# Performance work log

Measured on AMD Instinct MI355X. Metric: run time of the kernel, lower is better.

The kernel has to match this reference:

```python
import jax, jax.numpy as jnp
from jax import lax
import numpy as np

B, T, E, H = 64, 512, 1024, 1024

def setup_inputs() -> dict:
    key = jax.random.key(0)
    k1, k2, k3, k4, k5, k6 = jax.random.split(key, 6)
    s = 1.0 / np.sqrt(H)  # torch LSTM init scale
    embeddings = jax.random.normal(k1, (B, T, E), dtype=jnp.float32)
    seq_lengths = jax.random.randint(k2, (B,), 1, T + 1)
    W_ih = jax.random.uniform(k3, (4 * H, E), minval=-s, maxval=s, dtype=jnp.float32)
    W_hh = jax.random.uniform(k4, (4 * H, H), minval=-s, maxval=s, dtype=jnp.float32)
    b_ih = jax.random.uniform(k5, (4 * H,), minval=-s, maxval=s, dtype=jnp.float32)
    b_hh = jax.random.uniform(k6, (4 * H,), minval=-s, maxval=s, dtype=jnp.float32)
    return {"embeddings": embeddings, "seq_lengths": seq_lengths,
            "W_ih": W_ih, "W_hh": W_hh, "b_ih": b_ih, "b_hh": b_hh}

def _lstm_outputs(embeddings, W_ih, W_hh, b_ih, b_hh):
    x = jnp.swapaxes(embeddings, 0, 1)  # [T, B, E] (time-major, as nn.LSTM batch_first=False)
    # Hoist the input projection into one big GEMM: [T,B,4H]
    x_proj = jnp.einsum('tbe,ge->tbg', x, W_ih) + b_ih + b_hh

    def step(carry, xp):
        h, c = carry
        gates = xp + h @ W_hh.T                      # [B, 4H]
        i, f, g, o = jnp.split(gates, 4, axis=-1)    # torch gate order: i, f, g, o
        i = jax.nn.sigmoid(i)
        f = jax.nn.sigmoid(f)
        g = jnp.tanh(g)
        o = jax.nn.sigmoid(o)
        c = f * c + i * g
        h = o * jnp.tanh(c)
        return (h, c), h

    h0 = jnp.zeros((x.shape[1], W_hh.shape[1]), x.dtype)
    _, outs = lax.scan(step, (h0, h0), x_proj)       # outs: [T, B, H]
    return outs

def reference(embeddings, seq_lengths, W_ih, W_hh, b_ih, b_hh):
    outs = _lstm_outputs(embeddings, W_ih, W_hh, b_ih, b_hh)  # [T, B, H]
    t = outs.shape[0]
    idx = (seq_lengths - 1) % t                      # wraps like python negative indexing
    repr_ = outs[idx, jnp.arange(outs.shape[1])]     # [B, H]
    return repr_
```

## Files before the change

kernel.cpp:

```cpp
#include <hip/hip_runtime.h>
#include <stdint.h>


typedef _Float16 half8 __attribute__((ext_vector_type(8)));
typedef _Float16 half4_ __attribute__((ext_vector_type(4)));
typedef float f32x4 __attribute__((ext_vector_type(4)));
typedef unsigned int u32x4 __attribute__((ext_vector_type(4)));

#define T_SEQ 512

__global__ void k_f32_to_f16(const float* __restrict__ s, _Float16* __restrict__ d, int n4) {
  int i = blockIdx.x * blockDim.x + threadIdx.x;
  if (i >= n4) return;
  f32x4 v = ((const f32x4*)s)[i];
  half4_ h;
  h.x = (_Float16)v.x; h.y = (_Float16)v.y; h.z = (_Float16)v.z; h.w = (_Float16)v.w;
  ((half4_*)d)[i] = h;
}

__global__ void k_bias_sum(const float* __restrict__ a, const float* __restrict__ b,
                           float* __restrict__ o) {
  int i = blockIdx.x * blockDim.x + threadIdx.x;
  if (i < 4096) o[i] = a[i] + b[i];
}

__global__ __launch_bounds__(256, 2) void k_gemm_xproj(
    const _Float16* __restrict__ X, const _Float16* __restrict__ W,
    const float* __restrict__ bsum, _Float16* __restrict__ C) {
  __shared__ _Float16 As[128 * 64];
  __shared__ _Float16 Bs[128 * 64];
  const int bid = blockIdx.x;
  const int ntile = bid & 31, mtile = bid >> 5;
  const int tid = threadIdx.x;
  const int wave = tid >> 6, lane = tid & 63;
  const int wr = wave >> 1, wc = wave & 1;
  const int R0 = lane >> 3, cg = lane & 7;

  f32x4 acc[4][4];
#pragma unroll
  for (int m = 0; m < 4; m++)
#pragma unroll
    for (int n = 0; n < 4; n++) acc[m][n] = (f32x4){0.f, 0.f, 0.f, 0.f};

  for (int k0 = 0; k0 < 1024; k0 += 64) {
#pragma unroll
    for (int i = 0; i < 4; i++) {
      const int rr = (wave * 4 + i) * 8 + R0;
      const _Float16* ga = X + (size_t)(mtile * 128 + rr) * 1024 + k0 + ((cg ^ (rr & 7)) * 8);
      const _Float16* gb = W + (size_t)(ntile * 128 + rr) * 1024 + k0 + ((cg ^ (rr & 7)) * 8);
      __builtin_amdgcn_global_load_lds(
          (const __attribute__((address_space(1))) void*)ga,
          (__attribute__((address_space(3))) void*)((char*)As + (wave * 4 + i) * 1024), 16, 0, 0);
      __builtin_amdgcn_global_load_lds(
          (const __attribute__((address_space(1))) void*)gb,
          (__attribute__((address_space(3))) void*)((char*)Bs + (wave * 4 + i) * 1024), 16, 0, 0);
    }
    asm volatile("s_waitcnt vmcnt(0)" ::: "memory");
    __syncthreads();
#pragma unroll
    for (int kk = 0; kk < 2; kk++) {
      half8 af[4], bf[4];
#pragma unroll
      for (int m = 0; m < 4; m++) {
        int r = wr * 64 + m * 16 + (lane & 15);
        af[m] = *(const half8*)((const char*)As + r * 128 +
                                (((kk * 4 + (lane >> 4)) ^ (r & 7)) << 4));
      }
#pragma unroll
      for (int n = 0; n < 4; n++) {
        int r = wc * 64 + n * 16 + (lane & 15);
        bf[n] = *(const half8*)((const char*)Bs + r * 128 +
                                (((kk * 4 + (lane >> 4)) ^ (r & 7)) << 4));
      }
#pragma unroll
      for (int m = 0; m < 4; m++)
#pragma unroll
        for (int n = 0; n < 4; n++)
          acc[m][n] = __builtin_amdgcn_mfma_f32_16x16x32_f16(af[m], bf[n], acc[m][n], 0, 0, 0);
    }
    __syncthreads();
  }
#pragma unroll
  for (int n = 0; n < 4; n++) {
    int col = ntile * 128 + wc * 64 + n * 16 + (lane & 15);
    float bs = bsum[col];
#pragma unroll
    for (int m = 0; m < 4; m++)
#pragma unroll
      for (int q = 0; q < 4; q++) {
        int row = mtile * 128 + wr * 64 + m * 16 + (lane >> 4) * 4 + q;
        C[(size_t)row * 4096 + col] = (_Float16)(acc[m][n][q] + bs);
      }
  }
}

__global__ __launch_bounds__(256, 1) void k_lstm_rec(
    const _Float16* __restrict__ Whh,
    const _Float16* __restrict__ xproj,
    const int* __restrict__ seqlen,
    _Float16* __restrict__ hbuf,
    unsigned* __restrict__ flags,
    float* __restrict__ out) {
  __shared__ _Float16 h_lds[16 * 1024];
  __shared__ float gates[16 * 64];

  const int wg = blockIdx.x;
  const int g = wg >> 6, s = wg & 63;
  const int tid = threadIdx.x;
  const int wave = tid >> 6, lane = tid & 63;

  for (int i = tid; i < 4096; i += 256) ((uint64_t*)h_lds)[i] = 0ull;

  half8 wfrag[32];
  {
    const _Float16* wrow =
        Whh + (size_t)(1024 * wave + 16 * s + (lane & 15)) * 1024 + (lane >> 4) * 8;
#pragma unroll
    for (int kk = 0; kk < 32; kk++) wfrag[kk] = *(const half8*)(wrow + kk * 32);
  }

  int Lg = 1;
  for (int b = 0; b < 16; b++) {
    int L = seqlen[g * 16 + b];
    Lg = L > Lg ? L : Lg;
  }
  const int be = tid >> 4, ue = tid & 15;
  const int mylen = seqlen[g * 16 + be];
  float c_state = 0.f;

  const int bA = lane & 15;
  const int rowbase = bA * 2048;
  const int xorm = (bA & 7) << 4;

  __syncthreads();

  for (int t = 0; t < Lg; t++) {
    float xp[4];
#pragma unroll
    for (int q = 0; q < 4; q++) {
      int bl = (lane >> 4) * 4 + q;
      size_t row = (size_t)(g * 16 + bl) * T_SEQ + t;
      xp[q] = (float)xproj[row * 4096 + 1024 * wave + 16 * s + (lane & 15)];
    }
    if (t > 0) {
      const unsigned* fl = flags + (((size_t)g * 512 + (t - 1)) << 6);
      for (;;) {
        unsigned v = __hip_atomic_load(&fl[lane], __ATOMIC_RELAXED, __HIP_MEMORY_SCOPE_AGENT);
        if (__ballot(v != 0u) == ~0ull) break;
      }
      const _Float16* hsrc = hbuf + ((size_t)(t & 1)) * 65536 + (size_t)(g * 16) * 1024;
      u32x4 hv[8];
#pragma unroll
      for (int i = 0; i < 8; i++) {
        int ch = tid + (i << 8);
        asm volatile("global_load_dwordx4 %0, %1, off sc0 sc1"
                     : "=v"(hv[i]) : "v"(hsrc + ch * 8) : "memory");
      }
      asm volatile("s_waitcnt vmcnt(0)" ::: "memory");
#pragma unroll
      for (int i = 0; i < 8; i++) {
        int ch = tid + (i << 8);
        int b = ch >> 7, j = ch & 127;
        *(u32x4*)((char*)h_lds + b * 2048 + ((j ^ (b & 7)) << 4)) = hv[i];
      }
    }
    __syncthreads();

    f32x4 acc0 = (f32x4){0.f, 0.f, 0.f, 0.f};
    f32x4 acc1 = (f32x4){0.f, 0.f, 0.f, 0.f};
#pragma unroll
    for (int kk = 0; kk < 32; kk += 2) {
      half8 a0 = *(const half8*)((const char*)h_lds + rowbase +
                                 ((((kk + 0) * 4 + (lane >> 4)) << 4) ^ xorm));
      half8 a1 = *(const half8*)((const char*)h_lds + rowbase +
                                 ((((kk + 1) * 4 + (lane >> 4)) << 4) ^ xorm));
      acc0 = __builtin_amdgcn_mfma_f32_16x16x32_f16(a0, wfrag[kk], acc0, 0, 0, 0);
      acc1 = __builtin_amdgcn_mfma_f32_16x16x32_f16(a1, wfrag[kk + 1], acc1, 0, 0, 0);
    }
#pragma unroll
    for (int q = 0; q < 4; q++) {
      int bm = (lane >> 4) * 4 + q;
      gates[bm * 64 + wave * 16 + (lane & 15)] = (acc0[q] + acc1[q]) + xp[q];
    }
    __syncthreads();

    float iv = gates[be * 64 + ue];
    float fv = gates[be * 64 + 16 + ue];
    float gv = gates[be * 64 + 32 + ue];
    float ov = gates[be * 64 + 48 + ue];
    iv = 1.f / (1.f + __expf(-iv));
    fv = 1.f / (1.f + __expf(-fv));
    gv = 1.f - 2.f / (1.f + __expf(2.f * gv));
    ov = 1.f / (1.f + __expf(-ov));
    c_state = fv * c_state + iv * gv;
    float tc = 1.f - 2.f / (1.f + __expf(2.f * c_state));
    float hv = ov * tc;
    if (t + 1 == mylen) out[(size_t)(g * 16 + be) * 1024 + s * 16 + ue] = hv;

    _Float16 hf = (_Float16)hv;
    unsigned short hb;
    __builtin_memcpy(&hb, &hf, 2);
    __hip_atomic_store((unsigned short*)hbuf + ((size_t)((t + 1) & 1)) * 65536 +
                           (size_t)(g * 16 + be) * 1024 + s * 16 + ue,
                       hb, __ATOMIC_RELAXED, __HIP_MEMORY_SCOPE_AGENT);
    __syncthreads();
    if (tid == 0)
      __hip_atomic_store(&flags[(((size_t)g * 512 + t) << 6) + s], 1u, __ATOMIC_RELAXED,
                         __HIP_MEMORY_SCOPE_AGENT);
  }
}

extern "C" void kernel_launch(void* const* d_in, const int* in_sizes, int n_in, void* d_out,
                              int out_size, void* d_ws, size_t ws_size, hipStream_t stream) {
  const float* emb = (const float*)d_in[0];
  const int* slen = (const int*)d_in[1];
  const float* Wih = (const float*)d_in[2];
  const float* Whh = (const float*)d_in[3];
  const float* bih = (const float*)d_in[4];
  const float* bhh = (const float*)d_in[5];
  float* out = (float*)d_out;

  char* ws = (char*)d_ws;
  _Float16* xproj = (_Float16*)(ws + 0);
  _Float16* xf = (_Float16*)(ws + 268435456);
  _Float16* wihf = (_Float16*)(ws + 335544320);
  _Float16* whhf = (_Float16*)(ws + 343932928);
  float* bsum = (float*)(ws + 352321536);
  _Float16* hbuf = (_Float16*)(ws + 268435456);
  unsigned* flags = (unsigned*)(ws + 268697600);

  k_f32_to_f16<<<(8388608 + 255) / 256, 256, 0, stream>>>(emb, xf, 8388608);
  k_f32_to_f16<<<(1048576 + 255) / 256, 256, 0, stream>>>(Wih, wihf, 1048576);
  k_f32_to_f16<<<(1048576 + 255) / 256, 256, 0, stream>>>(Whh, whhf, 1048576);
  k_bias_sum<<<16, 256, 0, stream>>>(bih, bhh, bsum);
  k_gemm_xproj<<<8192, 256, 0, stream>>>(xf, wihf, bsum, xproj);
  hipMemsetAsync(flags, 0, 524288, stream);
  k_lstm_rec<<<256, 256, 0, stream>>>(whhf, xproj, slen, hbuf, flags, out);
}
```

Baseline: 2.073 ms.

## Replace flag barrier with step-tagged hidden-state words and halve recurrent workgroups

The recurrent kernel drops the separate per-step flag array. Each hidden value is now stored as a 32-bit word whose top 16 bits carry the timestep, so consumers poll the data itself until every tag matches, which removes the extra barrier and flag store per step. Workgroups grow to 512 threads covering 32 hidden units each, so 32 groups per batch slice synchronise instead of 64. The x-projection GEMM now writes its output time-major, giving the per-step gate-input loads better locality. In exchange, the polling traffic doubles because each hidden value now takes 4 bytes.

```diff
diff --git a/kernel.cpp b/kernel.cpp
--- a/kernel.cpp
+++ b/kernel.cpp
@@ -89,32 +89,33 @@
 #pragma unroll
       for (int q = 0; q < 4; q++) {
         int row = mtile * 128 + wr * 64 + m * 16 + (lane >> 4) * 4 + q;
-        C[(size_t)row * 4096 + col] = (_Float16)(acc[m][n][q] + bs);
-      }
-  }
-}
-
-__global__ __launch_bounds__(256, 1) void k_lstm_rec(
+        int bb = row >> 9, tt = row & 511;
+        C[((size_t)tt * 64 + bb) * 4096 + col] = (_Float16)(acc[m][n][q] + bs);
+      }
+  }
+}
+
+__global__ __launch_bounds__(512, 2) void k_lstm_rec(
     const _Float16* __restrict__ Whh,
-    const _Float16* __restrict__ xproj,
+    const _Float16* __restrict__ xprojT,
     const int* __restrict__ seqlen,
-    _Float16* __restrict__ hbuf,
-    unsigned* __restrict__ flags,
+    unsigned* __restrict__ hbuf,
     float* __restrict__ out) {
   __shared__ _Float16 h_lds[16 * 1024];
-  __shared__ float gates[16 * 64];
+  __shared__ float gates[16 * 132];
 
   const int wg = blockIdx.x;
-  const int g = wg >> 6, s = wg & 63;
+  const int g = wg >> 5, s2 = wg & 31;
   const int tid = threadIdx.x;
   const int wave = tid >> 6, lane = tid & 63;
-
-  for (int i = tid; i < 4096; i += 256) ((uint64_t*)h_lds)[i] = 0ull;
+  const int G = wave >> 1, uh = wave & 1;
+
+  for (int i = tid; i < 4096; i += 512) ((uint64_t*)h_lds)[i] = 0ull;
 
   half8 wfrag[32];
   {
     const _Float16* wrow =
-        Whh + (size_t)(1024 * wave + 16 * s + (lane & 15)) * 1024 + (lane >> 4) * 8;
+        Whh + (size_t)(1024 * G + s2 * 32 + uh * 16 + (lane & 15)) * 1024 + (lane >> 4) * 8;
 #pragma unroll
     for (int kk = 0; kk < 32; kk++) wfrag[kk] = *(const half8*)(wrow + kk * 32);
   }
@@ -124,13 +125,15 @@
     int L = seqlen[g * 16 + b];
     Lg = L > Lg ? L : Lg;
   }
-  const int be = tid >> 4, ue = tid & 15;
+  const int be = tid >> 5, ue = tid & 31;
   const int mylen = seqlen[g * 16 + be];
   float c_state = 0.f;
 
   const int bA = lane & 15;
   const int rowbase = bA * 2048;
   const int xorm = (bA & 7) << 4;
+  const int pb = tid >> 5;
+  const int pj = tid & 31;
 
   __syncthreads();
 
@@ -138,30 +141,38 @@
     float xp[4];
 #pragma unroll
     for (int q = 0; q < 4; q++) {
-      int bl = (lane >> 4) * 4 + q;
-      size_t row = (size_t)(g * 16 + bl) * T_SEQ + t;
-      xp[q] = (float)xproj[row * 4096 + 1024 * wave + 16 * s + (lane & 15)];
+      int bm = (lane >> 4) * 4 + q;
+      xp[q] = (float)xprojT[((size_t)t * 64 + g * 16 + bm) * 4096 + 1024 * G + s2 * 32 +
+                            uh * 16 + (lane & 15)];
     }
     if (t > 0) {
-      const unsigned* fl = flags + (((size_t)g * 512 + (t - 1)) << 6);
+      const unsigned* src = hbuf + ((size_t)(t & 1)) * 65536 + (size_t)(g * 16 + pb) * 1024;
+      u32x4 pv[8];
       for (;;) {
-        unsigned v = __hip_atomic_load(&fl[lane], __ATOMIC_RELAXED, __HIP_MEMORY_SCOPE_AGENT);
-        if (__ballot(v != 0u) == ~0ull) break;
-      }
-      const _Float16* hsrc = hbuf + ((size_t)(t & 1)) * 65536 + (size_t)(g * 16) * 1024;
-      u32x4 hv[8];
-#pragma unroll
-      for (int i = 0; i < 8; i++) {
-        int ch = tid + (i << 8);
-        asm volatile("global_load_dwordx4 %0, %1, off sc0 sc1"
-                     : "=v"(hv[i]) : "v"(hsrc + ch * 8) : "memory");
-      }
-      asm volatile("s_waitcnt vmcnt(0)" ::: "memory");
-#pragma unroll
-      for (int i = 0; i < 8; i++) {
-        int ch = tid + (i << 8);
-        int b = ch >> 7, j = ch & 127;
-        *(u32x4*)((char*)h_lds + b * 2048 + ((j ^ (b & 7)) << 4)) = hv[i];
+#pragma unroll
+        for (int i = 0; i < 4; i++) {
+          asm volatile("global_load_dwordx4 %0, %1, off sc0 sc1"
+                       : "=v"(pv[2 * i]) : "v"(src + (pj + 32 * i) * 8) : "memory");
+          asm volatile("global_load_dwordx4 %0, %1, off sc0 sc1"
+                       : "=v"(pv[2 * i + 1]) : "v"(src + (pj + 32 * i) * 8 + 4) : "memory");
+        }
+        asm volatile("s_waitcnt vmcnt(0)" ::: "memory");
+        bool ok = true;
+#pragma unroll
+        for (int i = 0; i < 8; i++)
+#pragma unroll
+          for (int d = 0; d < 4; d++) ok &= ((pv[i][d] >> 16) == (unsigned)t);
+        if (__all(ok)) break;
+      }
+#pragma unroll
+      for (int i = 0; i < 4; i++) {
+        u32x4 pk;
+        pk.x = (pv[2 * i].x & 0xffffu) | (pv[2 * i].y << 16);
+        pk.y = (pv[2 * i].z & 0xffffu) | (pv[2 * i].w << 16);
+        pk.z = (pv[2 * i + 1].x & 0xffffu) | (pv[2 * i + 1].y << 16);
+        pk.w = (pv[2 * i + 1].z & 0xffffu) | (pv[2 * i + 1].w << 16);
+        int j = pj + 32 * i;
+        *(u32x4*)((char*)h_lds + pb * 2048 + ((j ^ (pb & 7)) << 4)) = pk;
       }
     }
     __syncthreads();
@@ -180,14 +191,14 @@
 #pragma unroll
     for (int q = 0; q < 4; q++) {
       int bm = (lane >> 4) * 4 + q;
-      gates[bm * 64 + wave * 16 + (lane & 15)] = (acc0[q] + acc1[q]) + xp[q];
-    }
-    __syncthreads();
-
-    float iv = gates[be * 64 + ue];
-    float fv = gates[be * 64 + 16 + ue];
-    float gv = gates[be * 64 + 32 + ue];
-    float ov = gates[be * 64 + 48 + ue];
+      gates[bm * 132 + wave * 16 + (lane & 15)] = (acc0[q] + acc1[q]) + xp[q];
+    }
+    __syncthreads();
+
+    float iv = gates[be * 132 + ue];
+    float fv = gates[be * 132 + 32 + ue];
+    float gv = gates[be * 132 + 64 + ue];
+    float ov = gates[be * 132 + 96 + ue];
     iv = 1.f / (1.f + __expf(-iv));
     fv = 1.f / (1.f + __expf(-fv));
     gv = 1.f - 2.f / (1.f + __expf(2.f * gv));
@@ -195,18 +206,15 @@
     c_state = fv * c_state + iv * gv;
     float tc = 1.f - 2.f / (1.f + __expf(2.f * c_state));
     float hv = ov * tc;
-    if (t + 1 == mylen) out[(size_t)(g * 16 + be) * 1024 + s * 16 + ue] = hv;
+    if (t + 1 == mylen) out[(size_t)(g * 16 + be) * 1024 + s2 * 32 + ue] = hv;
 
     _Float16 hf = (_Float16)hv;
-    unsigned short hb;
-    __builtin_memcpy(&hb, &hf, 2);
-    __hip_atomic_store((unsigned short*)hbuf + ((size_t)((t + 1) & 1)) * 65536 +
-                           (size_t)(g * 16 + be) * 1024 + s * 16 + ue,
-                       hb, __ATOMIC_RELAXED, __HIP_MEMORY_SCOPE_AGENT);
-    __syncthreads();
-    if (tid == 0)
-      __hip_atomic_store(&flags[(((size_t)g * 512 + t) << 6) + s], 1u, __ATOMIC_RELAXED,
-                         __HIP_MEMORY_SCOPE_AGENT);
+    unsigned short hb16;
+    __builtin_memcpy(&hb16, &hf, 2);
+    unsigned tagword = ((unsigned)(t + 1) << 16) | (unsigned)hb16;
+    __hip_atomic_store(hbuf + ((size_t)((t + 1) & 1)) * 65536 + (size_t)(g * 16 + be) * 1024 +
+                           s2 * 32 + ue,
+                       tagword, __ATOMIC_RELAXED, __HIP_MEMORY_SCOPE_AGENT);
   }
 }
 
@@ -221,19 +229,18 @@
   float* out = (float*)d_out;
 
   char* ws = (char*)d_ws;
-  _Float16* xproj = (_Float16*)(ws + 0);
+  _Float16* xprojT = (_Float16*)(ws + 0);
   _Float16* xf = (_Float16*)(ws + 268435456);
   _Float16* wihf = (_Float16*)(ws + 335544320);
   _Float16* whhf = (_Float16*)(ws + 343932928);
   float* bsum = (float*)(ws + 352321536);
-  _Float16* hbuf = (_Float16*)(ws + 268435456);
-  unsigned* flags = (unsigned*)(ws + 268697600);
+  unsigned* hbuf = (unsigned*)(ws + 268435456);
 
   k_f32_to_f16<<<(8388608 + 255) / 256, 256, 0, stream>>>(emb, xf, 8388608);
   k_f32_to_f16<<<(1048576 + 255) / 256, 256, 0, stream>>>(Wih, wihf, 1048576);
   k_f32_to_f16<<<(1048576 + 255) / 256, 256, 0, stream>>>(Whh, whhf, 1048576);
   k_bias_sum<<<16, 256, 0, stream>>>(bih, bhh, bsum);
-  k_gemm_xproj<<<8192, 256, 0, stream>>>(xf, wihf, bsum, xproj);
-  hipMemsetAsync(flags, 0, 524288, stream);
-  k_lstm_rec<<<256, 256, 0, stream>>>(whhf, xproj, slen, hbuf, flags, out);
-}
+  k_gemm_xproj<<<8192, 256, 0, stream>>>(xf, wihf, bsum, xprojT);
+  hipMemsetAsync(hbuf, 0, 524288, stream);
+  k_lstm_rec<<<128, 512, 0, stream>>>(whhf, xprojT, slen, hbuf, out);
+}
```

New measurement: 2.983 ms. 1.44x slower.

## Remove LDS gate exchange via DPP, per-wave flags, time-major xproj, full h history

Applied to the files above, without the earlier changes.

Reorders W_hh rows so each MFMA output quad holds the i,f,g,o gates for one unit, and reads them with DPP lane broadcasts instead of a shared-memory gates buffer. This removes two block barriers per step. Each wave now publishes its own flag after a vmcnt wait, and consumers poll the flags with a single vector load. The h buffer keeps every timestep instead of ping-ponging between two slots, h in LDS is double-buffered, the xproj GEMM writes in time-major order for coalesced per-step reads, and workgroups are remapped across the grid. The cost is a larger flags and h workspace with a bigger memset, and the weakened ordering between the h stores and the flag stores needs care.

```diff
diff --git a/kernel.cpp b/kernel.cpp
--- a/kernel.cpp
+++ b/kernel.cpp
@@ -1,5 +1,6 @@
 #include <hip/hip_runtime.h>
 #include <stdint.h>
+#include <string.h>
 
 
 typedef _Float16 half8 __attribute__((ext_vector_type(8)));
@@ -89,34 +90,44 @@
 #pragma unroll
       for (int q = 0; q < 4; q++) {
         int row = mtile * 128 + wr * 64 + m * 16 + (lane >> 4) * 4 + q;
-        C[(size_t)row * 4096 + col] = (_Float16)(acc[m][n][q] + bs);
-      }
-  }
+        int bb = row >> 9, tt = row & 511;
+        C[((size_t)tt * 64 + bb) * 4096 + col] = (_Float16)(acc[m][n][q] + bs);
+      }
+  }
+}
+
+template <int CTRL>
+__device__ __forceinline__ float qb(float v) {
+  int i = __builtin_bit_cast(int, v);
+  i = __builtin_amdgcn_update_dpp(0, i, CTRL, 0xF, 0xF, false);
+  return __builtin_bit_cast(float, i);
 }
 
 __global__ __launch_bounds__(256, 1) void k_lstm_rec(
     const _Float16* __restrict__ Whh,
-    const _Float16* __restrict__ xproj,
+    const _Float16* __restrict__ xprojT,
     const int* __restrict__ seqlen,
     _Float16* __restrict__ hbuf,
     unsigned* __restrict__ flags,
     float* __restrict__ out) {
-  __shared__ _Float16 h_lds[16 * 1024];
-  __shared__ float gates[16 * 64];
-
-  const int wg = blockIdx.x;
-  const int g = wg >> 6, s = wg & 63;
+  __shared__ _Float16 h_lds[2][16 * 1024];
+
+  const int bid = blockIdx.x;
+  const int x8 = bid & 7;
+  const int g = x8 >> 1;
+  const int s = (x8 & 1) * 32 + (bid >> 3);
   const int tid = threadIdx.x;
   const int wave = tid >> 6, lane = tid & 63;
 
-  for (int i = tid; i < 4096; i += 256) ((uint64_t*)h_lds)[i] = 0ull;
-
+  for (int i = tid; i < 4096; i += 256) ((uint64_t*)h_lds[0])[i] = 0ull;
+
+  const int n = lane & 15;
   half8 wfrag[32];
   {
-    const _Float16* wrow =
-        Whh + (size_t)(1024 * wave + 16 * s + (lane & 15)) * 1024 + (lane >> 4) * 8;
-#pragma unroll
-    for (int kk = 0; kk < 32; kk++) wfrag[kk] = *(const half8*)(wrow + kk * 32);
+    const _Float16* wp =
+        Whh + (size_t)(1024 * (n & 3) + s * 16 + wave * 4 + (n >> 2)) * 1024 + (lane >> 4) * 8;
+#pragma unroll
+    for (int kk = 0; kk < 32; kk++) wfrag[kk] = *(const half8*)(wp + kk * 32);
   }
 
   int Lg = 1;
@@ -124,13 +135,15 @@
     int L = seqlen[g * 16 + b];
     Lg = L > Lg ? L : Lg;
   }
-  const int be = tid >> 4, ue = tid & 15;
-  const int mylen = seqlen[g * 16 + be];
-  float c_state = 0.f;
-
-  const int bA = lane & 15;
-  const int rowbase = bA * 2048;
-  const int xorm = (bA & 7) << 4;
+  const int bm_st = (lane >> 4) * 4 + (lane & 3);
+  const int mylen_st = seqlen[g * 16 + bm_st];
+  const int unitF = s * 16 + wave * 4 + ((lane >> 2) & 3);
+  const int colF = 1024 * (lane & 3) + unitF;
+
+  const int rowbase = (lane & 15) * 2048;
+  const int xorm = ((lane & 15) & 7) << 4;
+
+  float cst[4] = {0.f, 0.f, 0.f, 0.f};
 
   __syncthreads();
 
@@ -138,75 +151,75 @@
     float xp[4];
 #pragma unroll
     for (int q = 0; q < 4; q++) {
-      int bl = (lane >> 4) * 4 + q;
-      size_t row = (size_t)(g * 16 + bl) * T_SEQ + t;
-      xp[q] = (float)xproj[row * 4096 + 1024 * wave + 16 * s + (lane & 15)];
-    }
+      int bm = (lane >> 4) * 4 + q;
+      xp[q] = (float)xprojT[((size_t)t * 64 + g * 16 + bm) * 4096 + colF];
+    }
+
     if (t > 0) {
-      const unsigned* fl = flags + (((size_t)g * 512 + (t - 1)) << 6);
+      const unsigned* fl = flags + (((size_t)t * 4 + g) << 8) + lane * 4;
+      u32x4 fv;
       for (;;) {
-        unsigned v = __hip_atomic_load(&fl[lane], __ATOMIC_RELAXED, __HIP_MEMORY_SCOPE_AGENT);
-        if (__ballot(v != 0u) == ~0ull) break;
-      }
-      const _Float16* hsrc = hbuf + ((size_t)(t & 1)) * 65536 + (size_t)(g * 16) * 1024;
+        asm volatile("global_load_dwordx4 %0, %1, off sc0 sc1"
+                     : "=v"(fv) : "v"(fl) : "memory");
+        asm volatile("s_waitcnt vmcnt(0)" ::: "memory");
+        bool ok = fv.x != 0u && fv.y != 0u && fv.z != 0u && fv.w != 0u;
+        if (__all(ok)) break;
+      }
+      const u32x4* src = (const u32x4*)(hbuf + (size_t)t * 65536 + (size_t)g * 16384);
       u32x4 hv[8];
 #pragma unroll
-      for (int i = 0; i < 8; i++) {
-        int ch = tid + (i << 8);
-        asm volatile("global_load_dwordx4 %0, %1, off sc0 sc1"
-                     : "=v"(hv[i]) : "v"(hsrc + ch * 8) : "memory");
-      }
-      asm volatile("s_waitcnt vmcnt(0)" ::: "memory");
+      for (int i = 0; i < 8; i++) hv[i] = src[tid + (i << 8)];
 #pragma unroll
       for (int i = 0; i < 8; i++) {
         int ch = tid + (i << 8);
         int b = ch >> 7, j = ch & 127;
-        *(u32x4*)((char*)h_lds + b * 2048 + ((j ^ (b & 7)) << 4)) = hv[i];
+        *(u32x4*)((char*)h_lds[t & 1] + b * 2048 + ((j ^ (b & 7)) << 4)) = hv[i];
       }
     }
     __syncthreads();
 
-    f32x4 acc0 = (f32x4){0.f, 0.f, 0.f, 0.f};
-    f32x4 acc1 = (f32x4){0.f, 0.f, 0.f, 0.f};
+    f32x4 a0 = (f32x4){0.f, 0.f, 0.f, 0.f};
+    f32x4 a1 = (f32x4){0.f, 0.f, 0.f, 0.f};
+    const char* lb = (const char*)h_lds[t & 1] + rowbase;
 #pragma unroll
     for (int kk = 0; kk < 32; kk += 2) {
-      half8 a0 = *(const half8*)((const char*)h_lds + rowbase +
-                                 ((((kk + 0) * 4 + (lane >> 4)) << 4) ^ xorm));
-      half8 a1 = *(const half8*)((const char*)h_lds + rowbase +
-                                 ((((kk + 1) * 4 + (lane >> 4)) << 4) ^ xorm));
-      acc0 = __builtin_amdgcn_mfma_f32_16x16x32_f16(a0, wfrag[kk], acc0, 0, 0, 0);
-      acc1 = __builtin_amdgcn_mfma_f32_16x16x32_f16(a1, wfrag[kk + 1], acc1, 0, 0, 0);
-    }
+      half8 f0 = *(const half8*)(lb + ((((kk + 0) * 4 + (lane >> 4)) << 4) ^ xorm));
+      half8 f1 = *(const half8*)(lb + ((((kk + 1) * 4 + (lane >> 4)) << 4) ^ xorm));
+      a0 = __builtin_amdgcn_mfma_f32_16x16x32_f16(f0, wfrag[kk + 0], a0, 0, 0, 0);
+      a1 = __builtin_amdgcn_mfma_f32_16x16x32_f16(f1, wfrag[kk + 1], a1, 0, 0, 0);
+    }
+
+    float hq[4];
 #pragma unroll
     for (int q = 0; q < 4; q++) {
-      int bm = (lane >> 4) * 4 + q;
-      gates[bm * 64 + wave * 16 + (lane & 15)] = (acc0[q] + acc1[q]) + xp[q];
-    }
-    __syncthreads();
-
-    float iv = gates[be * 64 + ue];
-    float fv = gates[be * 64 + 16 + ue];
-    float gv = gates[be * 64 + 32 + ue];
-    float ov = gates[be * 64 + 48 + ue];
-    iv = 1.f / (1.f + __expf(-iv));
-    fv = 1.f / (1.f + __expf(-fv));
-    gv = 1.f - 2.f / (1.f + __expf(2.f * gv));
-    ov = 1.f / (1.f + __expf(-ov));
-    c_state = fv * c_state + iv * gv;
-    float tc = 1.f - 2.f / (1.f + __expf(2.f * c_state));
-    float hv = ov * tc;
-    if (t + 1 == mylen) out[(size_t)(g * 16 + be) * 1024 + s * 16 + ue] = hv;
-
-    _Float16 hf = (_Float16)hv;
-    unsigned short hb;
-    __builtin_memcpy(&hb, &hf, 2);
-    __hip_atomic_store((unsigned short*)hbuf + ((size_t)((t + 1) & 1)) * 65536 +
-                           (size_t)(g * 16 + be) * 1024 + s * 16 + ue,
-                       hb, __ATOMIC_RELAXED, __HIP_MEMORY_SCOPE_AGENT);
-    __syncthreads();
-    if (tid == 0)
-      __hip_atomic_store(&flags[(((size_t)g * 512 + t) << 6) + s], 1u, __ATOMIC_RELAXED,
-                         __HIP_MEMORY_SCOPE_AGENT);
+      float val = (a0[q] + a1[q]) + xp[q];
+      float iv = qb<0x00>(val);
+      float fg = qb<0x55>(val);
+      float gv = qb<0xAA>(val);
+      float ov = qb<0xFF>(val);
+      iv = 1.f / (1.f + __expf(-iv));
+      fg = 1.f / (1.f + __expf(-fg));
+      gv = 1.f - 2.f / (1.f + __expf(2.f * gv));
+      ov = 1.f / (1.f + __expf(-ov));
+      cst[q] = fg * cst[q] + iv * gv;
+      hq[q] = ov * (1.f - 2.f / (1.f + __expf(2.f * cst[q])));
+    }
+    const int m = lane & 3;
+    float hsel = m == 0 ? hq[0] : (m == 1 ? hq[1] : (m == 2 ? hq[2] : hq[3]));
+    if (t + 1 == mylen_st) out[(size_t)(g * 16 + bm_st) * 1024 + unitF] = hsel;
+
+    if (t + 1 < Lg) {
+      _Float16 hf = (_Float16)hsel;
+      unsigned short hb;
+      __builtin_memcpy(&hb, &hf, 2);
+      __hip_atomic_store((unsigned short*)hbuf + (size_t)(t + 1) * 65536 +
+                             (size_t)(g * 16 + bm_st) * 1024 + unitF,
+                         hb, __ATOMIC_RELAXED, __HIP_MEMORY_SCOPE_AGENT);
+      asm volatile("s_waitcnt vmcnt(0)" ::: "memory");
+      if (lane == 0)
+        __hip_atomic_store(&flags[(((size_t)(t + 1) * 4 + g) << 8) + s * 4 + wave], 1u,
+                           __ATOMIC_RELAXED, __HIP_MEMORY_SCOPE_AGENT);
+    }
   }
 }
 
@@ -221,19 +234,19 @@
   float* out = (float*)d_out;
 
   char* ws = (char*)d_ws;
-  _Float16* xproj = (_Float16*)(ws + 0);
+  _Float16* xprojT = (_Float16*)(ws + 0);
   _Float16* xf = (_Float16*)(ws + 268435456);
-  _Float16* wihf = (_Float16*)(ws + 335544320);
-  _Float16* whhf = (_Float16*)(ws + 343932928);
-  float* bsum = (float*)(ws + 352321536);
   _Float16* hbuf = (_Float16*)(ws + 268435456);
-  unsigned* flags = (unsigned*)(ws + 268697600);
-
+  _Float16* wihf = (_Float16*)(ws + 335675392);
+  _Float16* whhf = (_Float16*)(ws + 344064000);
+  float* bsum = (float*)(ws + 352452608);
+  unsigned* flags = (unsigned*)(ws + 352468992);
+
+  hipMemsetAsync(flags, 0, 2101248, stream);
   k_f32_to_f16<<<(8388608 + 255) / 256, 256, 0, stream>>>(emb, xf, 8388608);
   k_f32_to_f16<<<(1048576 + 255) / 256, 256, 0, stream>>>(Wih, wihf, 1048576);
   k_f32_to_f16<<<(1048576 + 255) / 256, 256, 0, stream>>>(Whh, whhf, 1048576);
   k_bias_sum<<<16, 256, 0, stream>>>(bih, bhh, bsum);
-  k_gemm_xproj<<<8192, 256, 0, stream>>>(xf, wihf, bsum, xproj);
-  hipMemsetAsync(flags, 0, 524288, stream);
-  k_lstm_rec<<<256, 256, 0, stream>>>(whhf, xproj, slen, hbuf, flags, out);
-}
+  k_gemm_xproj<<<8192, 256, 0, stream>>>(xf, wihf, bsum, xprojT);
+  k_lstm_rec<<<256, 256, 0, stream>>>(whhf, xprojT, slen, hbuf, flags, out);
+}
```

After: 4.686 ms. +126.0%, slower.
